# Kernel optimization log

Hardware: AMD Instinct MI355X
Metric: run time of the kernel (lower is better)

The kernel has to match this reference:

```python
import jax, jax.numpy as jnp
import numpy as np

R, N, B = 3, 8192, 4096
IN_DIM, HID, OUT = 256, 128, 64
EPS = 1e-5


def _bn(x, g, b):
    # BatchNorm1d in training mode: biased batch stats over dim 0
    m = jnp.mean(x, axis=0)
    v = jnp.var(x, axis=0)
    return (x - m) * jax.lax.rsqrt(v + EPS) * g + b


def setup_inputs() -> dict:
    key = jax.random.key(0)
    k1, k2, k3, k4, k5 = jax.random.split(key, 5)
    features = jax.random.normal(k1, (N, IN_DIM), dtype=jnp.float32)
    u = jax.random.uniform(k2, (R, N, N), dtype=jnp.float32)
    adj = (u < 0.01).astype(jnp.float32)
    batch_nodes = jax.random.randint(k3, (B,), 0, N, dtype=jnp.int32)
    w1 = jax.random.uniform(k4, (IN_DIM, HID), dtype=jnp.float32)  # torch.rand init
    w2 = jax.random.uniform(k5, (HID, OUT), dtype=jnp.float32)
    return {
        "features": features, "adj": adj, "batch_nodes": batch_nodes,
        "w1": w1, "w2": w2,
        "gamma1": jnp.ones((IN_DIM,), jnp.float32), "beta1": jnp.zeros((IN_DIM,), jnp.float32),
        "gamma2": jnp.ones((OUT,), jnp.float32), "beta2": jnp.zeros((OUT,), jnp.float32),
    }


def reference(features, adj, batch_nodes, w1, w2, gamma1, beta1, gamma2, beta2):
    # gather batch subgraph
    x = features[batch_nodes]                       # [B, IN_DIM]
    bA = jnp.take(jnp.take(adj, batch_nodes, axis=1), batch_nodes, axis=2)  # [R, B, B]
    xn = _bn(x, gamma1, beta1)                      # shared across relations

    def per_relation(badj):
        A = badj + jnp.eye(B, dtype=badj.dtype)
        # D_mx.inverse().sqrt() of a diagonal degree matrix == diag(deg^-1/2)
        dinv = jax.lax.rsqrt(jnp.sum(A, axis=1))    # [B]
        A_hat = A * dinv[:, None] * dinv[None, :]   # D^-1/2 A D^-1/2
        h1 = jax.nn.sigmoid(jax.nn.elu((A_hat @ xn) @ w1))   # conv1 + sigmoid
        h2 = jax.nn.elu((A_hat @ h1) @ w2)                   # conv2
        return _bn(h2, gamma2, beta2)

    embed = jax.vmap(per_relation)(bA)              # [R, B, OUT]
    return jax.nn.relu(jnp.mean(embed, axis=0))     # [B, OUT]
```

## Files before the change

kernel.cpp:

```cpp
#include <hip/hip_runtime.h>
#include <hip/hip_bf16.h>

#define RR 3
#define NN 8192
#define BB 4096
#define IN_DIM 256
#define HID 128
#define OUT 64
#define CAPD 128
#define EPS 1e-5f
#define MWN (NN / 64)
#define MLPB 16

__global__ __launch_bounds__(1024) void prep_k(const int* __restrict__ bn,
                                               unsigned long long* __restrict__ memb,
                                               unsigned short* __restrict__ rankg,
                                               unsigned short* __restrict__ nodeof,
                                               float* __restrict__ multf,
                                               int* __restrict__ Ucnt,
                                               unsigned short* __restrict__ pos2slot) {
    __shared__ int smult[NN];
    __shared__ unsigned short srank[NN];
    __shared__ unsigned long long smemb[MWN];
    __shared__ int sbase[MWN + 1];
    int t = threadIdx.x;
    for (int u = t; u < NN; u += 1024) smult[u] = 0;
    __syncthreads();
    for (int i = t; i < BB; i += 1024) atomicAdd(&smult[bn[i]], 1);
    __syncthreads();
    if (t < MWN) {
        unsigned long long w = 0;
        for (int b = 0; b < 64; ++b) if (smult[t * 64 + b]) w |= (1ull << b);
        smemb[t] = w;
        memb[t] = w;
    }
    __syncthreads();
    if (t == 0) {
        int acc = 0;
        for (int m = 0; m < MWN; ++m) { sbase[m] = acc; acc += (int)__popcll(smemb[m]); }
        sbase[MWN] = acc;
        *Ucnt = acc;
    }
    __syncthreads();
    if (t < MWN) {
        unsigned long long w = smemb[t];
        int p = sbase[t];
        while (w) {
            int b = __builtin_ctzll(w); w &= w - 1;
            int u = t * 64 + b;
            srank[u] = (unsigned short)p;
            rankg[u] = (unsigned short)p;
            nodeof[p] = (unsigned short)u;
            multf[p]  = (float)smult[u];
            ++p;
        }
    }
    __syncthreads();
    for (int i = t; i < BB; i += 1024) pos2slot[i] = srank[bn[i]];
}

__global__ __launch_bounds__(256) void bn1_stats_k(const float* __restrict__ feat,
                                                   const int* __restrict__ bn,
                                                   float* __restrict__ m1,
                                                   float* __restrict__ rs1) {
    int c = blockIdx.x;
    float s = 0.f, q = 0.f;
    for (int i = threadIdx.x; i < BB; i += 256) {
        float v = feat[(size_t)bn[i] * IN_DIM + c];
        s += v; q += v * v;
    }
    int lane = threadIdx.x & 63, wv = threadIdx.x >> 6;
    for (int o = 32; o; o >>= 1) { s += __shfl_down(s, o); q += __shfl_down(q, o); }
    __shared__ float ps[4], pq[4];
    if (lane == 0) { ps[wv] = s; pq[wv] = q; }
    __syncthreads();
    if (threadIdx.x == 0) {
        float S = ps[0] + ps[1] + ps[2] + ps[3];
        float Q = pq[0] + pq[1] + pq[2] + pq[3];
        float m = S / BB;
        float v = Q / BB - m * m;
        m1[c] = m;
        rs1[c] = rsqrtf(v + EPS);
    }
}

__global__ __launch_bounds__(256) void xn_c_k(const float* __restrict__ feat,
                                              const unsigned short* __restrict__ nodeof,
                                              const int* __restrict__ Ucnt,
                                              const float* __restrict__ m1,
                                              const float* __restrict__ rs1,
                                              const float* __restrict__ g1,
                                              const float* __restrict__ b1,
                                              float* __restrict__ xn_c) {
    int s = blockIdx.x;
    if (s >= *Ucnt) return;
    int u = nodeof[s];
    int c = threadIdx.x;
    float v = feat[(size_t)u * IN_DIM + c];
    xn_c[(size_t)s * IN_DIM + c] = (v - m1[c]) * rs1[c] * g1[c] + b1[c];
}

__global__ __launch_bounds__(256) void build_k(const float* __restrict__ adj,
                                               const unsigned short* __restrict__ nodeof,
                                               const int* __restrict__ Ucnt,
                                               const unsigned long long* __restrict__ memb,
                                               const unsigned short* __restrict__ rankg,
                                               const float* __restrict__ multf,
                                               unsigned short* __restrict__ cols,
                                               int* __restrict__ cnt,
                                               float* __restrict__ dinv) {
    int blk = blockIdx.x;
    int r = blk >> 12, s = blk & (BB - 1);
    if (s >= *Ucnt) return;
    int u = nodeof[s];
    __shared__ unsigned char nib[2048];
    __shared__ unsigned int rawb[256];
    __shared__ unsigned long long sel[MWN];
    __shared__ int sbase[MWN + 1];
    __shared__ float pdeg[4];
    int t = threadIdx.x;
    const float4* ar4 = (const float4*)(adj + ((size_t)r * NN + u) * NN);
    #pragma unroll
    for (int ch = 0; ch < 8; ++ch) {
        float4 v = ar4[ch * 256 + t];
        nib[ch * 256 + t] = (unsigned char)((v.x != 0.f) | ((v.y != 0.f) << 1) |
                                            ((v.z != 0.f) << 2) | ((v.w != 0.f) << 3));
    }
    __syncthreads();
    {
        unsigned long long x = *(const unsigned long long*)&nib[t * 8];
        x = (x | (x >> 4))  & 0x00FF00FF00FF00FFull;
        x = (x | (x >> 8))  & 0x0000FFFF0000FFFFull;
        x = (x | (x >> 16));
        rawb[t] = (unsigned int)x;
    }
    __syncthreads();
    if (t < MWN) {
        unsigned long long w = ((unsigned long long)rawb[2 * t + 1] << 32) | rawb[2 * t];
        sel[t] = w & memb[t];
    }
    __syncthreads();
    if (t < 64) {
        int p0 = (int)__popcll(sel[2 * t]);
        int p1 = (int)__popcll(sel[2 * t + 1]);
        int x = p0 + p1, xs = x;
        for (int o = 1; o < 64; o <<= 1) { int y = __shfl_up(xs, o); if (t >= o) xs += y; }
        sbase[2 * t]     = xs - x;
        sbase[2 * t + 1] = xs - p1;
        if (t == 63) sbase[MWN] = xs;
    }
    __syncthreads();
    float wdeg = 0.f;
    if (t < MWN) {
        unsigned long long w = sel[t];
        int p = sbase[t];
        unsigned short* cb = cols + (size_t)blk * CAPD;
        while (w) {
            int b = __builtin_ctzll(w); w &= w - 1;
            int v = t * 64 + b;
            int rv = rankg[v];
            if (p < CAPD) cb[p] = (unsigned short)rv;
            wdeg += multf[rv];
            ++p;
        }
    }
    int lane = t & 63, wv = t >> 6;
    for (int o = 32; o; o >>= 1) wdeg += __shfl_down(wdeg, o);
    if (lane == 0) pdeg[wv] = wdeg;
    __syncthreads();
    if (t == 0) {
        int tot = sbase[MWN];
        cnt[blk] = tot < CAPD ? tot : CAPD;
        dinv[blk] = rsqrtf(pdeg[0] + pdeg[1] + pdeg[2] + pdeg[3] + 1.0f);
    }
}

__global__ __launch_bounds__(256) void layer1_agg_k(const float* __restrict__ xn_c,
                                                    const unsigned short* __restrict__ cols,
                                                    const int* __restrict__ cnt,
                                                    const float* __restrict__ dinv,
                                                    const float* __restrict__ multf,
                                                    const int* __restrict__ Ucnt,
                                                    float* __restrict__ y1) {
    int blk = blockIdx.x;
    int r = blk >> 12, s = blk & (BB - 1);
    if (s >= *Ucnt) return;
    int c = threadIdx.x;
    __shared__ unsigned short scl[CAPD];
    __shared__ float swl[CAPD];
    int n = cnt[blk];
    if (c < n) {
        int sl = cols[(size_t)blk * CAPD + c];
        scl[c] = (unsigned short)sl;
        swl[c] = multf[sl] * dinv[(r << 12) + sl];
    }
    __syncthreads();
    float di = dinv[blk];
    float acc = di * xn_c[(size_t)s * IN_DIM + c];
    #pragma unroll 4
    for (int k = 0; k < n; ++k) {
        acc += swl[k] * xn_c[(size_t)scl[k] * IN_DIM + c];
    }
    y1[(size_t)blk * IN_DIM + c] = acc * di;
}

__global__ __launch_bounds__(256) void mlp1_k(const float* __restrict__ y1,
                                              const int* __restrict__ Ucnt,
                                              const float* __restrict__ w1,
                                              float* __restrict__ h1) {
    int blk = blockIdx.x;
    int r = blk / (BB / MLPB), base = (blk % (BB / MLPB)) * MLPB;
    int U = *Ucnt;
    if (base >= U) return;
    int t = threadIdx.x;
    __shared__ float ys[MLPB][IN_DIM];
    #pragma unroll
    for (int s = 0; s < MLPB; ++s) {
        int slot = base + s;
        ys[s][t] = (slot < U) ? y1[((size_t)(r << 12) + slot) * IN_DIM + t] : 0.f;
    }
    __syncthreads();
    int c = t & 127, g = t >> 7;
    float acc[8] = {0.f};
    for (int k = 0; k < IN_DIM; ++k) {
        float wv = w1[k * HID + c];
        #pragma unroll
        for (int j = 0; j < 8; ++j) acc[j] += ys[g * 8 + j][k] * wv;
    }
    #pragma unroll
    for (int j = 0; j < 8; ++j) {
        int slot = base + g * 8 + j;
        if (slot < U) {
            float z = acc[j];
            float e = z > 0.f ? z : expm1f(z);
            h1[((size_t)(r << 12) + slot) * HID + c] = 1.f / (1.f + expf(-e));
        }
    }
}

__global__ __launch_bounds__(128) void layer2_agg_k(const float* __restrict__ h1,
                                                    const unsigned short* __restrict__ cols,
                                                    const int* __restrict__ cnt,
                                                    const float* __restrict__ dinv,
                                                    const float* __restrict__ multf,
                                                    const int* __restrict__ Ucnt,
                                                    float* __restrict__ y2) {
    int blk = blockIdx.x;
    int r = blk >> 12, s = blk & (BB - 1);
    if (s >= *Ucnt) return;
    int c = threadIdx.x;
    __shared__ unsigned short scl[CAPD];
    __shared__ float swl[CAPD];
    int n = cnt[blk];
    if (c < n) {
        int sl = cols[(size_t)blk * CAPD + c];
        scl[c] = (unsigned short)sl;
        swl[c] = multf[sl] * dinv[(r << 12) + sl];
    }
    __syncthreads();
    const float* h1r = h1 + ((size_t)(r << 12)) * HID;
    float di = dinv[blk];
    float acc = di * h1r[(size_t)s * HID + c];
    #pragma unroll 4
    for (int k = 0; k < n; ++k) {
        acc += swl[k] * h1r[(size_t)scl[k] * HID + c];
    }
    y2[(size_t)blk * HID + c] = acc * di;
}

__global__ __launch_bounds__(256) void mlp2_k(const float* __restrict__ y2,
                                              const int* __restrict__ Ucnt,
                                              const float* __restrict__ w2,
                                              float* __restrict__ h2) {
    int blk = blockIdx.x;
    int r = blk / (BB / MLPB), base = (blk % (BB / MLPB)) * MLPB;
    int U = *Ucnt;
    if (base >= U) return;
    int t = threadIdx.x;
    __shared__ float ys[MLPB][HID];
    #pragma unroll
    for (int s = t >> 7; s < MLPB; s += 2) {
        int slot = base + s;
        ys[s][t & 127] = (slot < U) ? y2[((size_t)(r << 12) + slot) * HID + (t & 127)] : 0.f;
    }
    __syncthreads();
    int c = t & 63, g = t >> 6;
    float acc[4] = {0.f};
    for (int k = 0; k < HID; ++k) {
        float wv = w2[k * OUT + c];
        #pragma unroll
        for (int j = 0; j < 4; ++j) acc[j] += ys[g * 4 + j][k] * wv;
    }
    #pragma unroll
    for (int j = 0; j < 4; ++j) {
        int slot = base + g * 4 + j;
        if (slot < U) {
            float z = acc[j];
            h2[((size_t)(r << 12) + slot) * OUT + c] = z > 0.f ? z : expm1f(z);
        }
    }
}

__global__ __launch_bounds__(256) void bn2_stats_k(const float* __restrict__ h2,
                                                   const float* __restrict__ multf,
                                                   const int* __restrict__ Ucnt,
                                                   float* __restrict__ m2,
                                                   float* __restrict__ rs2) {
    int ro = blockIdx.x;
    int r = ro >> 6, o = ro & (OUT - 1);
    int U = *Ucnt;
    float s = 0.f, q = 0.f;
    for (int sl = threadIdx.x; sl < U; sl += 256) {
        float m = multf[sl];
        float v = h2[(size_t)((r << 12) + sl) * OUT + o];
        s += m * v; q += m * v * v;
    }
    int lane = threadIdx.x & 63, wv = threadIdx.x >> 6;
    for (int off = 32; off; off >>= 1) { s += __shfl_down(s, off); q += __shfl_down(q, off); }
    __shared__ float ps[4], pq[4];
    if (lane == 0) { ps[wv] = s; pq[wv] = q; }
    __syncthreads();
    if (threadIdx.x == 0) {
        float S = ps[0] + ps[1] + ps[2] + ps[3];
        float Q = pq[0] + pq[1] + pq[2] + pq[3];
        float m = S / BB;
        float v = Q / BB - m * m;
        m2[ro] = m;
        rs2[ro] = rsqrtf(v + EPS);
    }
}

__global__ __launch_bounds__(256) void finalize_k(const float* __restrict__ h2,
                                                  const unsigned short* __restrict__ pos2slot,
                                                  const float* __restrict__ m2,
                                                  const float* __restrict__ rs2,
                                                  const float* __restrict__ g2,
                                                  const float* __restrict__ b2,
                                                  float* __restrict__ out) {
    int idx = blockIdx.x * 256 + threadIdx.x;
    if (idx >= BB * OUT) return;
    int i = idx >> 6, o = idx & (OUT - 1);
    int sl = pos2slot[i];
    float s = 0.f;
    for (int r = 0; r < RR; ++r) {
        float v = h2[(size_t)((r << 12) + sl) * OUT + o];
        s += (v - m2[r * OUT + o]) * rs2[r * OUT + o] * g2[o] + b2[o];
    }
    s *= (1.0f / RR);
    out[idx] = s > 0.f ? s : 0.f;
}

extern "C" void kernel_launch(void* const* d_in, const int* in_sizes, int n_in,
                              void* d_out, int out_size, void* d_ws, size_t ws_size,
                              hipStream_t stream) {
    const float* feat = (const float*)d_in[0];
    const float* adj  = (const float*)d_in[1];
    const int*   bn   = (const int*)d_in[2];
    const float* w1   = (const float*)d_in[3];
    const float* w2   = (const float*)d_in[4];
    const float* g1   = (const float*)d_in[5];
    const float* b1   = (const float*)d_in[6];
    const float* g2   = (const float*)d_in[7];
    const float* b2   = (const float*)d_in[8];
    float* out = (float*)d_out;

    char* ws = (char*)d_ws;
    size_t off = 0;
    auto alloc = [&](size_t bytes) { size_t o = off; off += (bytes + 255) & ~(size_t)255; return o; };
    unsigned long long* memb = (unsigned long long*)(ws + alloc(MWN * 8));
    unsigned short* rankg    = (unsigned short*)(ws + alloc(NN * 2));
    unsigned short* nodeof   = (unsigned short*)(ws + alloc(BB * 2));
    float* multf             = (float*)(ws + alloc(BB * 4));
    int* Ucnt                = (int*)(ws + alloc(4));
    unsigned short* pos2slot = (unsigned short*)(ws + alloc(BB * 2));
    float* m1                = (float*)(ws + alloc(IN_DIM * 4));
    float* rs1               = (float*)(ws + alloc(IN_DIM * 4));
    float* m2                = (float*)(ws + alloc(RR * OUT * 4));
    float* rs2               = (float*)(ws + alloc(RR * OUT * 4));
    float* xn_c              = (float*)(ws + alloc((size_t)BB * IN_DIM * 4));
    unsigned short* cols     = (unsigned short*)(ws + alloc((size_t)RR * BB * CAPD * 2));
    int* cnt                 = (int*)(ws + alloc((size_t)RR * BB * 4));
    float* dinv              = (float*)(ws + alloc((size_t)RR * BB * 4));
    float* y1                = (float*)(ws + alloc((size_t)RR * BB * IN_DIM * 4));
    float* h1                = (float*)(ws + alloc((size_t)RR * BB * HID * 4));
    float* y2                = (float*)(ws + alloc((size_t)RR * BB * HID * 4));
    float* h2                = (float*)(ws + alloc((size_t)RR * BB * OUT * 4));

    prep_k<<<1, 1024, 0, stream>>>(bn, memb, rankg, nodeof, multf, Ucnt, pos2slot);
    bn1_stats_k<<<IN_DIM, 256, 0, stream>>>(feat, bn, m1, rs1);
    xn_c_k<<<BB, 256, 0, stream>>>(feat, nodeof, Ucnt, m1, rs1, g1, b1, xn_c);
    build_k<<<RR * BB, 256, 0, stream>>>(adj, nodeof, Ucnt, memb, rankg, multf, cols, cnt, dinv);
    layer1_agg_k<<<RR * BB, 256, 0, stream>>>(xn_c, cols, cnt, dinv, multf, Ucnt, y1);
    mlp1_k<<<RR * (BB / MLPB), 256, 0, stream>>>(y1, Ucnt, w1, h1);
    layer2_agg_k<<<RR * BB, 128, 0, stream>>>(h1, cols, cnt, dinv, multf, Ucnt, y2);
    mlp2_k<<<RR * (BB / MLPB), 256, 0, stream>>>(y2, Ucnt, w2, h2);
    bn2_stats_k<<<RR * OUT, 256, 0, stream>>>(h2, multf, Ucnt, m2, rs2);
    finalize_k<<<(BB * OUT + 255) / 256, 256, 0, stream>>>(h2, pos2slot, m2, rs2, g2, b2, out);
}
```

Before: 172.1 us.

## Vectorize aggregation and MLP kernels and split BN1 statistics into two passes

BN1 statistics now use a two-stage reduction: 64 blocks load float4 rows from the gathered features and write partial sums, and a small kernel finishes the mean and rsqrt. Both aggregation kernels pack the neighbor index and weight into one shared uint2, process two neighbors per iteration and load float2 per thread with half the threads. The MLP kernels are register-tiled so each thread computes a 2-row by 4- or 2-column output block from float4 shared-memory and weight loads. Together these aim to cut instruction count and uncoalesced scalar loads. The cost is an extra kernel launch and MLP work on padding rows past the unique count.

After: 184.6 us. +7.3%, slower.

```diff
diff --git a/kernel.cpp b/kernel.cpp
--- a/kernel.cpp
+++ b/kernel.cpp
@@ -59,29 +59,46 @@
     for (int i = t; i < BB; i += 1024) pos2slot[i] = srank[bn[i]];
 }
 
-__global__ __launch_bounds__(256) void bn1_stats_k(const float* __restrict__ feat,
-                                                   const int* __restrict__ bn,
-                                                   float* __restrict__ m1,
-                                                   float* __restrict__ rs1) {
-    int c = blockIdx.x;
-    float s = 0.f, q = 0.f;
-    for (int i = threadIdx.x; i < BB; i += 256) {
-        float v = feat[(size_t)bn[i] * IN_DIM + c];
-        s += v; q += v * v;
-    }
-    int lane = threadIdx.x & 63, wv = threadIdx.x >> 6;
-    for (int o = 32; o; o >>= 1) { s += __shfl_down(s, o); q += __shfl_down(q, o); }
-    __shared__ float ps[4], pq[4];
-    if (lane == 0) { ps[wv] = s; pq[wv] = q; }
-    __syncthreads();
-    if (threadIdx.x == 0) {
-        float S = ps[0] + ps[1] + ps[2] + ps[3];
-        float Q = pq[0] + pq[1] + pq[2] + pq[3];
-        float m = S / BB;
-        float v = Q / BB - m * m;
-        m1[c] = m;
-        rs1[c] = rsqrtf(v + EPS);
-    }
+__global__ __launch_bounds__(256) void bn1p_k(const float* __restrict__ feat,
+                                              const int* __restrict__ bn,
+                                              float* __restrict__ partial) {
+    int b = blockIdx.x;
+    int t = threadIdx.x;
+    int g = t >> 6, c4 = (t & 63) << 2;
+    float4 s = make_float4(0.f, 0.f, 0.f, 0.f), q = s;
+    for (int it = 0; it < 16; ++it) {
+        int i = b * 64 + g * 16 + it;
+        const float4 v = *(const float4*)(feat + (size_t)bn[i] * IN_DIM + c4);
+        s.x += v.x; s.y += v.y; s.z += v.z; s.w += v.w;
+        q.x += v.x * v.x; q.y += v.y * v.y; q.z += v.z * v.z; q.w += v.w * v.w;
+    }
+    __shared__ float4 rs_[4][64], rq_[4][64];
+    rs_[g][t & 63] = s; rq_[g][t & 63] = q;
+    __syncthreads();
+    if (t < 64) {
+        float4 S = rs_[0][t], Q = rq_[0][t];
+        for (int gg = 1; gg < 4; ++gg) {
+            float4 a = rs_[gg][t], bq = rq_[gg][t];
+            S.x += a.x; S.y += a.y; S.z += a.z; S.w += a.w;
+            Q.x += bq.x; Q.y += bq.y; Q.z += bq.z; Q.w += bq.w;
+        }
+        *(float4*)(partial + ((size_t)(2 * b) * IN_DIM) + t * 4) = S;
+        *(float4*)(partial + ((size_t)(2 * b + 1) * IN_DIM) + t * 4) = Q;
+    }
+}
+
+__global__ __launch_bounds__(256) void bn1f_k(const float* __restrict__ partial,
+                                              float* __restrict__ m1,
+                                              float* __restrict__ rs1) {
+    int c = threadIdx.x;
+    float S = 0.f, Q = 0.f;
+    for (int b = 0; b < 64; ++b) {
+        S += partial[(size_t)(2 * b) * IN_DIM + c];
+        Q += partial[(size_t)(2 * b + 1) * IN_DIM + c];
+    }
+    float m = S / BB;
+    m1[c] = m;
+    rs1[c] = rsqrtf(Q / BB - m * m + EPS);
 }
 
 __global__ __launch_bounds__(256) void xn_c_k(const float* __restrict__ feat,
@@ -175,33 +192,41 @@
     }
 }
 
-__global__ __launch_bounds__(256) void layer1_agg_k(const float* __restrict__ xn_c,
-                                                    const unsigned short* __restrict__ cols,
-                                                    const int* __restrict__ cnt,
-                                                    const float* __restrict__ dinv,
-                                                    const float* __restrict__ multf,
-                                                    const int* __restrict__ Ucnt,
-                                                    float* __restrict__ y1) {
+__global__ __launch_bounds__(128) void agg1_k(const float* __restrict__ xn_c,
+                                              const unsigned short* __restrict__ cols,
+                                              const int* __restrict__ cnt,
+                                              const float* __restrict__ dinv,
+                                              const float* __restrict__ multf,
+                                              const int* __restrict__ Ucnt,
+                                              float* __restrict__ y1) {
     int blk = blockIdx.x;
     int r = blk >> 12, s = blk & (BB - 1);
     if (s >= *Ucnt) return;
     int c = threadIdx.x;
-    __shared__ unsigned short scl[CAPD];
-    __shared__ float swl[CAPD];
+    __shared__ __align__(16) uint2 swp[CAPD];
     int n = cnt[blk];
     if (c < n) {
         int sl = cols[(size_t)blk * CAPD + c];
-        scl[c] = (unsigned short)sl;
-        swl[c] = multf[sl] * dinv[(r << 12) + sl];
-    }
+        swp[c] = make_uint2((unsigned)sl, __float_as_uint(multf[sl] * dinv[(r << 12) + sl]));
+    }
+    if (c == n && n < CAPD) swp[c] = make_uint2(0u, 0u);
     __syncthreads();
     float di = dinv[blk];
-    float acc = di * xn_c[(size_t)s * IN_DIM + c];
-    #pragma unroll 4
-    for (int k = 0; k < n; ++k) {
-        acc += swl[k] * xn_c[(size_t)scl[k] * IN_DIM + c];
-    }
-    y1[(size_t)blk * IN_DIM + c] = acc * di;
+    float2 v = ((const float2*)(xn_c + (size_t)s * IN_DIM))[c];
+    float ax = di * v.x, ay = di * v.y;
+    int nn = (n + 1) & ~1;
+    const uint4* sw4 = (const uint4*)swp;
+    #pragma unroll 2
+    for (int kk = 0; kk < (nn >> 1); ++kk) {
+        uint4 e = sw4[kk];
+        float w0 = __uint_as_float(e.y), w1v = __uint_as_float(e.w);
+        float2 x0 = ((const float2*)(xn_c + (size_t)e.x * IN_DIM))[c];
+        float2 x1 = ((const float2*)(xn_c + (size_t)e.z * IN_DIM))[c];
+        ax += w0 * x0.x + w1v * x1.x;
+        ay += w0 * x0.y + w1v * x1.y;
+    }
+    float2 o = make_float2(ax * di, ay * di);
+    *(float2*)(y1 + (size_t)blk * IN_DIM + c * 2) = o;
 }
 
 __global__ __launch_bounds__(256) void mlp1_k(const float* __restrict__ y1,
@@ -209,63 +234,84 @@
                                               const float* __restrict__ w1,
                                               float* __restrict__ h1) {
     int blk = blockIdx.x;
-    int r = blk / (BB / MLPB), base = (blk % (BB / MLPB)) * MLPB;
+    int r = blk >> 8, base = (blk & 255) * MLPB;
     int U = *Ucnt;
     if (base >= U) return;
     int t = threadIdx.x;
     __shared__ float ys[MLPB][IN_DIM];
     #pragma unroll
-    for (int s = 0; s < MLPB; ++s) {
-        int slot = base + s;
-        ys[s][t] = (slot < U) ? y1[((size_t)(r << 12) + slot) * IN_DIM + t] : 0.f;
-    }
-    __syncthreads();
-    int c = t & 127, g = t >> 7;
-    float acc[8] = {0.f};
-    for (int k = 0; k < IN_DIM; ++k) {
-        float wv = w1[k * HID + c];
-        #pragma unroll
-        for (int j = 0; j < 8; ++j) acc[j] += ys[g * 8 + j][k] * wv;
-    }
-    #pragma unroll
-    for (int j = 0; j < 8; ++j) {
-        int slot = base + g * 8 + j;
-        if (slot < U) {
-            float z = acc[j];
-            float e = z > 0.f ? z : expm1f(z);
-            h1[((size_t)(r << 12) + slot) * HID + c] = 1.f / (1.f + expf(-e));
-        }
-    }
-}
-
-__global__ __launch_bounds__(128) void layer2_agg_k(const float* __restrict__ h1,
-                                                    const unsigned short* __restrict__ cols,
-                                                    const int* __restrict__ cnt,
-                                                    const float* __restrict__ dinv,
-                                                    const float* __restrict__ multf,
-                                                    const int* __restrict__ Ucnt,
-                                                    float* __restrict__ y2) {
+    for (int s = 0; s < MLPB; ++s)
+        ys[s][t] = y1[((size_t)(r << 12) + base + s) * IN_DIM + t];
+    __syncthreads();
+    int p = t >> 5;
+    int c4 = (t & 31) << 2;
+    float4 a0c = make_float4(0.f,0.f,0.f,0.f), a1c = a0c;
+    for (int k = 0; k < IN_DIM; k += 4) {
+        float4 a0 = *(const float4*)&ys[2 * p][k];
+        float4 a1 = *(const float4*)&ys[2 * p + 1][k];
+        float4 w0 = *(const float4*)(w1 + (size_t)(k + 0) * HID + c4);
+        float4 wv1 = *(const float4*)(w1 + (size_t)(k + 1) * HID + c4);
+        float4 wv2 = *(const float4*)(w1 + (size_t)(k + 2) * HID + c4);
+        float4 wv3 = *(const float4*)(w1 + (size_t)(k + 3) * HID + c4);
+        a0c.x += a0.x*w0.x + a0.y*wv1.x + a0.z*wv2.x + a0.w*wv3.x;
+        a0c.y += a0.x*w0.y + a0.y*wv1.y + a0.z*wv2.y + a0.w*wv3.y;
+        a0c.z += a0.x*w0.z + a0.y*wv1.z + a0.z*wv2.z + a0.w*wv3.z;
+        a0c.w += a0.x*w0.w + a0.y*wv1.w + a0.z*wv2.w + a0.w*wv3.w;
+        a1c.x += a1.x*w0.x + a1.y*wv1.x + a1.z*wv2.x + a1.w*wv3.x;
+        a1c.y += a1.x*w0.y + a1.y*wv1.y + a1.z*wv2.y + a1.w*wv3.y;
+        a1c.z += a1.x*w0.z + a1.y*wv1.z + a1.z*wv2.z + a1.w*wv3.z;
+        a1c.w += a1.x*w0.w + a1.y*wv1.w + a1.z*wv2.w + a1.w*wv3.w;
+    }
+    float* o0 = h1 + ((size_t)(r << 12) + base + 2 * p) * HID + c4;
+    float* o1 = o0 + HID;
+    float4 r0, r1;
+    #define ACT1(zz) (1.f / (1.f + expf(-((zz) > 0.f ? (zz) : expm1f(zz)))))
+    r0.x = ACT1(a0c.x); r0.y = ACT1(a0c.y); r0.z = ACT1(a0c.z); r0.w = ACT1(a0c.w);
+    r1.x = ACT1(a1c.x); r1.y = ACT1(a1c.y); r1.z = ACT1(a1c.z); r1.w = ACT1(a1c.w);
+    #undef ACT1
+    *(float4*)o0 = r0;
+    *(float4*)o1 = r1;
+}
+
+__global__ __launch_bounds__(64) void agg2_k(const float* __restrict__ h1,
+                                             const unsigned short* __restrict__ cols,
+                                             const int* __restrict__ cnt,
+                                             const float* __restrict__ dinv,
+                                             const float* __restrict__ multf,
+                                             const int* __restrict__ Ucnt,
+                                             float* __restrict__ y2) {
     int blk = blockIdx.x;
     int r = blk >> 12, s = blk & (BB - 1);
     if (s >= *Ucnt) return;
     int c = threadIdx.x;
-    __shared__ unsigned short scl[CAPD];
-    __shared__ float swl[CAPD];
+    __shared__ __align__(16) uint2 swp[CAPD];
     int n = cnt[blk];
-    if (c < n) {
-        int sl = cols[(size_t)blk * CAPD + c];
-        scl[c] = (unsigned short)sl;
-        swl[c] = multf[sl] * dinv[(r << 12) + sl];
+    int nn = (n + 1) & ~1;
+    for (int idx = c; idx < nn; idx += 64) {
+        if (idx < n) {
+            int sl = cols[(size_t)blk * CAPD + idx];
+            swp[idx] = make_uint2((unsigned)sl, __float_as_uint(multf[sl] * dinv[(r << 12) + sl]));
+        } else {
+            swp[idx] = make_uint2(0u, 0u);
+        }
     }
     __syncthreads();
     const float* h1r = h1 + ((size_t)(r << 12)) * HID;
     float di = dinv[blk];
-    float acc = di * h1r[(size_t)s * HID + c];
-    #pragma unroll 4
-    for (int k = 0; k < n; ++k) {
-        acc += swl[k] * h1r[(size_t)scl[k] * HID + c];
-    }
-    y2[(size_t)blk * HID + c] = acc * di;
+    float2 v = ((const float2*)(h1r + (size_t)s * HID))[c];
+    float ax = di * v.x, ay = di * v.y;
+    const uint4* sw4 = (const uint4*)swp;
+    #pragma unroll 2
+    for (int kk = 0; kk < (nn >> 1); ++kk) {
+        uint4 e = sw4[kk];
+        float w0 = __uint_as_float(e.y), w1v = __uint_as_float(e.w);
+        float2 x0 = ((const float2*)(h1r + (size_t)e.x * HID))[c];
+        float2 x1 = ((const float2*)(h1r + (size_t)e.z * HID))[c];
+        ax += w0 * x0.x + w1v * x1.x;
+        ay += w0 * x0.y + w1v * x1.y;
+    }
+    float2 o = make_float2(ax * di, ay * di);
+    *(float2*)(y2 + (size_t)blk * HID + c * 2) = o;
 }
 
 __global__ __launch_bounds__(256) void mlp2_k(const float* __restrict__ y2,
@@ -273,32 +319,42 @@
                                               const float* __restrict__ w2,
                                               float* __restrict__ h2) {
     int blk = blockIdx.x;
-    int r = blk / (BB / MLPB), base = (blk % (BB / MLPB)) * MLPB;
+    int r = blk >> 8, base = (blk & 255) * MLPB;
     int U = *Ucnt;
     if (base >= U) return;
     int t = threadIdx.x;
     __shared__ float ys[MLPB][HID];
-    #pragma unroll
-    for (int s = t >> 7; s < MLPB; s += 2) {
-        int slot = base + s;
-        ys[s][t & 127] = (slot < U) ? y2[((size_t)(r << 12) + slot) * HID + (t & 127)] : 0.f;
-    }
-    __syncthreads();
-    int c = t & 63, g = t >> 6;
-    float acc[4] = {0.f};
-    for (int k = 0; k < HID; ++k) {
-        float wv = w2[k * OUT + c];
+    {
+        int s2 = t >> 7, cc = t & 127;
         #pragma unroll
-        for (int j = 0; j < 4; ++j) acc[j] += ys[g * 4 + j][k] * wv;
-    }
-    #pragma unroll
-    for (int j = 0; j < 4; ++j) {
-        int slot = base + g * 4 + j;
-        if (slot < U) {
-            float z = acc[j];
-            h2[((size_t)(r << 12) + slot) * OUT + c] = z > 0.f ? z : expm1f(z);
-        }
-    }
+        for (int s = s2; s < MLPB; s += 2)
+            ys[s][cc] = y2[((size_t)(r << 12) + base + s) * HID + cc];
+    }
+    __syncthreads();
+    int p = t >> 5;
+    int c2 = (t & 31) << 1;
+    float2 a0c = make_float2(0.f, 0.f), a1c = a0c;
+    for (int k = 0; k < HID; k += 4) {
+        float4 a0 = *(const float4*)&ys[2 * p][k];
+        float4 a1 = *(const float4*)&ys[2 * p + 1][k];
+        float2 w0 = *(const float2*)(w2 + (size_t)(k + 0) * OUT + c2);
+        float2 wv1 = *(const float2*)(w2 + (size_t)(k + 1) * OUT + c2);
+        float2 wv2 = *(const float2*)(w2 + (size_t)(k + 2) * OUT + c2);
+        float2 wv3 = *(const float2*)(w2 + (size_t)(k + 3) * OUT + c2);
+        a0c.x += a0.x*w0.x + a0.y*wv1.x + a0.z*wv2.x + a0.w*wv3.x;
+        a0c.y += a0.x*w0.y + a0.y*wv1.y + a0.z*wv2.y + a0.w*wv3.y;
+        a1c.x += a1.x*w0.x + a1.y*wv1.x + a1.z*wv2.x + a1.w*wv3.x;
+        a1c.y += a1.x*w0.y + a1.y*wv1.y + a1.z*wv2.y + a1.w*wv3.y;
+    }
+    float* o0 = h2 + ((size_t)(r << 12) + base + 2 * p) * OUT + c2;
+    float* o1 = o0 + OUT;
+    float2 r0, r1;
+    r0.x = a0c.x > 0.f ? a0c.x : expm1f(a0c.x);
+    r0.y = a0c.y > 0.f ? a0c.y : expm1f(a0c.y);
+    r1.x = a1c.x > 0.f ? a1c.x : expm1f(a1c.x);
+    r1.y = a1c.y > 0.f ? a1c.y : expm1f(a1c.y);
+    *(float2*)o0 = r0;
+    *(float2*)o1 = r1;
 }
 
 __global__ __launch_bounds__(256) void bn2_stats_k(const float* __restrict__ h2,
@@ -373,6 +429,7 @@
     float* multf             = (float*)(ws + alloc(BB * 4));
     int* Ucnt                = (int*)(ws + alloc(4));
     unsigned short* pos2slot = (unsigned short*)(ws + alloc(BB * 2));
+    float* partial           = (float*)(ws + alloc(128 * IN_DIM * 4));
     float* m1                = (float*)(ws + alloc(IN_DIM * 4));
     float* rs1               = (float*)(ws + alloc(IN_DIM * 4));
     float* m2                = (float*)(ws + alloc(RR * OUT * 4));
@@ -387,13 +444,14 @@
     float* h2                = (float*)(ws + alloc((size_t)RR * BB * OUT * 4));
 
     prep_k<<<1, 1024, 0, stream>>>(bn, memb, rankg, nodeof, multf, Ucnt, pos2slot);
-    bn1_stats_k<<<IN_DIM, 256, 0, stream>>>(feat, bn, m1, rs1);
+    bn1p_k<<<64, 256, 0, stream>>>(feat, bn, partial);
+    bn1f_k<<<1, 256, 0, stream>>>(partial, m1, rs1);
     xn_c_k<<<BB, 256, 0, stream>>>(feat, nodeof, Ucnt, m1, rs1, g1, b1, xn_c);
     build_k<<<RR * BB, 256, 0, stream>>>(adj, nodeof, Ucnt, memb, rankg, multf, cols, cnt, dinv);
-    layer1_agg_k<<<RR * BB, 256, 0, stream>>>(xn_c, cols, cnt, dinv, multf, Ucnt, y1);
-    mlp1_k<<<RR * (BB / MLPB), 256, 0, stream>>>(y1, Ucnt, w1, h1);
-    layer2_agg_k<<<RR * BB, 128, 0, stream>>>(h1, cols, cnt, dinv, multf, Ucnt, y2);
-    mlp2_k<<<RR * (BB / MLPB), 256, 0, stream>>>(y2, Ucnt, w2, h2);
+    agg1_k<<<RR * BB, 128, 0, stream>>>(xn_c, cols, cnt, dinv, multf, Ucnt, y1);
+    mlp1_k<<<RR * 256, 256, 0, stream>>>(y1, Ucnt, w1, h1);
+    agg2_k<<<RR * BB, 64, 0, stream>>>(h1, cols, cnt, dinv, multf, Ucnt, y2);
+    mlp2_k<<<RR * 256, 256, 0, stream>>>(y2, Ucnt, w2, h2);
     bn2_stats_k<<<RR * OUT, 256, 0, stream>>>(h2, multf, Ucnt, m2, rs2);
     finalize_k<<<(BB * OUT + 255) / 256, 256, 0, stream>>>(h2, pos2slot, m2, rs2, g2, b2, out);
 }
```
